# Optimization experiments

Hardware: AMD Instinct MI355X
Metric: run time of the kernel (lower is better)

Reference implementation:

```python
import jax, jax.numpy as jnp
import numpy as np

EMBED = 512
HEADS = 8
SCALE = 4
B, N = 2, 2048
DH = EMBED // HEADS
EPS = 1e-5


def _mha(q_in, k_in, v_in, wq, bq, wk, bk, wv, bv, wo, bo, causal):
    Bq, Nq, _ = q_in.shape
    Nk = k_in.shape[1]
    Q = (q_in @ wq + bq).reshape(Bq, Nq, HEADS, DH)
    K = (k_in @ wk + bk).reshape(Bq, Nk, HEADS, DH)
    V = (v_in @ wv + bv).reshape(Bq, Nk, HEADS, DH)
    # scores: [B, H, Nq, Nk]
    scores = jnp.einsum('bqhd,bkhd->bhqk', Q, K) / np.sqrt(DH).astype(np.float32)
    if causal:
        mask = jnp.triu(jnp.full((Nq, Nq), -jnp.inf, dtype=scores.dtype), k=1)
        scores = scores + mask[None, None]
    attn = jax.nn.softmax(scores, axis=-1)
    out = jnp.einsum('bhqk,bkhd->bqhd', attn, V).reshape(Bq, Nq, EMBED)
    return out @ wo + bo


def _ln(x, g, b):
    mu = jnp.mean(x, axis=-1, keepdims=True)
    var = jnp.var(x, axis=-1, keepdims=True)
    return (x - mu) * jax.lax.rsqrt(var + EPS) * g + b


def setup_inputs() -> dict:
    key = jax.random.key(0)
    ks = iter(jax.random.split(key, 32))
    p = lambda *s: 0.02 * jax.random.normal(next(ks), s, dtype=jnp.float32)
    inp = {
        'x': jax.random.normal(next(ks), (B, N, EMBED), dtype=jnp.float32),
        'encoder_output': jax.random.normal(next(ks), (B, N, EMBED), dtype=jnp.float32),
    }
    for pre in ('sa', 'ca'):
        inp[pre + '_wq'] = p(EMBED, EMBED); inp[pre + '_bq'] = jnp.zeros(EMBED)
        inp[pre + '_wk'] = p(EMBED, EMBED); inp[pre + '_bk'] = jnp.zeros(EMBED)
        inp[pre + '_wv'] = p(EMBED, EMBED); inp[pre + '_bv'] = jnp.zeros(EMBED)
        inp[pre + '_wo'] = p(EMBED, EMBED); inp[pre + '_bo'] = jnp.zeros(EMBED)
    for i in (1, 2, 3):
        inp[f'ln{i}_g'] = jnp.ones(EMBED); inp[f'ln{i}_b'] = jnp.zeros(EMBED)
    inp['ff_w1'] = p(EMBED, SCALE * EMBED); inp['ff_b1'] = jnp.zeros(SCALE * EMBED)
    inp['ff_w2'] = p(SCALE * EMBED, EMBED); inp['ff_b2'] = jnp.zeros(EMBED)
    return inp


def reference(x, encoder_output,
              sa_wq, sa_bq, sa_wk, sa_bk, sa_wv, sa_bv, sa_wo, sa_bo,
              ca_wq, ca_bq, ca_wk, ca_bk, ca_wv, ca_bv, ca_wo, ca_bo,
              ln1_g, ln1_b, ln2_g, ln2_b, ln3_g, ln3_b,
              ff_w1, ff_b1, ff_w2, ff_b2):
    x = _mha(x, x, x, sa_wq, sa_bq, sa_wk, sa_bk, sa_wv, sa_bv, sa_wo, sa_bo, True) + x
    x = _ln(x, ln1_g, ln1_b)
    x = _mha(x, encoder_output, encoder_output,
             ca_wq, ca_bq, ca_wk, ca_bk, ca_wv, ca_bv, ca_wo, ca_bo, False) + x
    x = _ln(x, ln2_g, ln2_b)
    h = jax.nn.gelu(x @ ff_w1 + ff_b1, approximate=False)
    x = h @ ff_w2 + ff_b2 + x
    return _ln(x, ln3_g, ln3_b)
```

## Files before the change

### kernel.cpp

```cpp
#include <hip/hip_runtime.h>
#include <hip/hip_bf16.h>

typedef __bf16 bf16x8 __attribute__((ext_vector_type(8)));
typedef float f32x4 __attribute__((ext_vector_type(4)));
typedef unsigned short u16;

#define EMB 512
#define FF 2048
#define MTOT 4096
#define SEQ 2048

__device__ __forceinline__ u16 f2b(float f) {
  return __builtin_bit_cast(u16, (__bf16)f);
}

__device__ __forceinline__ int swz64(int row) { return ((row >> 3) ^ row) & 7; }

__device__ __forceinline__ void gload16(const u16* g, u16* l) {
  __builtin_amdgcn_global_load_lds(
      (const __attribute__((address_space(1))) unsigned int*)g,
      (__attribute__((address_space(3))) unsigned int*)l, 16, 0, 0);
}

__global__ __launch_bounds__(256) void prep_all(
    const float* s0, const float* s1, const float* s2, const float* s3,
    const float* s4, const float* s5, const float* s6, const float* s7,
    const float* s8, const float* s9,
    u16* d0, u16* d1, u16* d2, u16* d3, u16* d4,
    u16* d5, u16* d6, u16* d7, u16* d8, u16* d9,
    const float* x, u16* xb, const float* enc, u16* encb,
    const float* bq1, const float* bk1, const float* bv1, float* bqkv,
    const float* bk2, const float* bv2, float* bkv) {
  int z = blockIdx.z, bx = blockIdx.x, by = blockIdx.y;
  int tid = threadIdx.x;
  if (z >= 10) {
    int fb = by * 64 + bx;
    const float* src = (z == 10) ? x : enc;
    u16* dst = (z == 10) ? xb : encb;
    size_t base = (size_t)fb * 2048 + tid * 8;
    float4 a = *(const float4*)(src + base);
    float4 b = *(const float4*)(src + base + 4);
    uint4 u;
    u.x = f2b(a.x) | ((unsigned)f2b(a.y) << 16);
    u.y = f2b(a.z) | ((unsigned)f2b(a.w) << 16);
    u.z = f2b(b.x) | ((unsigned)f2b(b.y) << 16);
    u.w = f2b(b.z) | ((unsigned)f2b(b.w) << 16);
    *(uint4*)(dst + base) = u;
    return;
  }
  if (z == 0 && bx == 16 && by == 0) {
    for (int i = tid; i < 1536; i += 256)
      bqkv[i] = (i < 512) ? bq1[i] : (i < 1024 ? bk1[i - 512] : bv1[i - 1024]);
    return;
  }
  if (z == 1 && bx == 16 && by == 0) {
    for (int i = tid; i < 1024; i += 256)
      bkv[i] = (i < 512) ? bk2[i] : bv2[i - 512];
    return;
  }
  const float* src; u16* dst; int K, N;
  switch (z) {
    case 0: src = s0; dst = d0; K = 512; N = 512; break;
    case 1: src = s1; dst = d1; K = 512; N = 512; break;
    case 2: src = s2; dst = d2; K = 512; N = 512; break;
    case 3: src = s3; dst = d3; K = 512; N = 512; break;
    case 4: src = s4; dst = d4; K = 512; N = 512; break;
    case 5: src = s5; dst = d5; K = 512; N = 512; break;
    case 6: src = s6; dst = d6; K = 512; N = 512; break;
    case 7: src = s7; dst = d7; K = 512; N = 512; break;
    case 8: src = s8; dst = d8; K = 512; N = 2048; break;
    default: src = s9; dst = d9; K = 2048; N = 512; break;
  }
  int ntl, ktl;
  if (z == 9) { ktl = bx; ntl = by; } else { ntl = bx; ktl = by; }
  if (ntl * 32 >= N || ktl * 32 >= K) return;
  __shared__ float t[32][33];
  int tx = tid & 31, ty = tid >> 5;
  int n0 = ntl * 32, k0 = ktl * 32;
#pragma unroll
  for (int i = 0; i < 4; i++)
    t[ty + i * 8][tx] = src[(size_t)(k0 + ty + i * 8) * N + n0 + tx];
  __syncthreads();
#pragma unroll
  for (int i = 0; i < 4; i++)
    dst[(size_t)(n0 + ty + i * 8) * K + k0 + tx] = f2b(t[tx][ty + i * 8]);
}

template <bool OUTB, bool OUTF, bool RES, bool GELU_>
__global__ __launch_bounds__(256) void gemm_bt(
    const u16* __restrict__ A, const u16* __restrict__ Bt,
    const float* __restrict__ bias, const float* __restrict__ resid,
    u16* __restrict__ outb, float* __restrict__ outf, int K, int Nd) {
  __shared__ u16 As[128 * 32];
  __shared__ u16 Bs[128 * 32];
  int tid = threadIdx.x;
  int lane = tid & 63, w = tid >> 6;
  int g = lane >> 4, li = lane & 15;
  int wr = w >> 1, wc = w & 1;
  int m0 = blockIdx.x * 128, n0 = blockIdx.y * 128;
  int row_s = tid >> 2, ch_s = tid & 3;
  int cs = ch_s ^ ((row_s ^ (row_s >> 2)) & 3);
  const u16* Ap = A + (size_t)(m0 + row_s) * K + cs * 8;
  const u16* Bp = Bt + (size_t)(n0 + row_s) * K + cs * 8;
  size_t step64 = (size_t)64 * K;
  int s2a = (li ^ (li >> 2)) & 3;
  f32x4 acc[4][4] = {};
  for (int k0 = 0; k0 < K; k0 += 32) {
    __syncthreads();
    gload16(Ap + k0, &As[w * 512]);
    gload16(Ap + step64 + k0, &As[2048 + w * 512]);
    gload16(Bp + k0, &Bs[w * 512]);
    gload16(Bp + step64 + k0, &Bs[2048 + w * 512]);
    __syncthreads();
    bf16x8 af[4], bfr[4];
#pragma unroll
    for (int i = 0; i < 4; i++) {
      af[i] = *(const bf16x8*)&As[(wr * 64 + i * 16 + li) * 32 + (g ^ s2a) * 8];
      bfr[i] = *(const bf16x8*)&Bs[(wc * 64 + i * 16 + li) * 32 + (g ^ s2a) * 8];
    }
#pragma unroll
    for (int mi = 0; mi < 4; mi++)
#pragma unroll
      for (int ni = 0; ni < 4; ni++)
        acc[mi][ni] = __builtin_amdgcn_mfma_f32_16x16x32_bf16(af[mi], bfr[ni], acc[mi][ni], 0, 0, 0);
  }
#pragma unroll
  for (int mi = 0; mi < 4; mi++)
#pragma unroll
    for (int ni = 0; ni < 4; ni++) {
      int gn = n0 + wc * 64 + ni * 16 + li;
      float bv = bias[gn];
#pragma unroll
      for (int r = 0; r < 4; r++) {
        int gm = m0 + wr * 64 + mi * 16 + g * 4 + r;
        float v = acc[mi][ni][r] + bv;
        if (RES) v += resid[(size_t)gm * Nd + gn];
        if (GELU_) v = 0.5f * v * (1.0f + erff(v * 0.70710678118654752f));
        if (OUTF) outf[(size_t)gm * Nd + gn] = v;
        if (OUTB) outb[(size_t)gm * Nd + gn] = f2b(v);
      }
    }
}

template <bool CAUSAL>
__global__ __launch_bounds__(256) void attn_fwd(
    const u16* __restrict__ Q, const u16* __restrict__ Kp,
    const u16* __restrict__ Vp, u16* __restrict__ O, int qs, int kvs) {
  __shared__ u16 Ks[64 * 64];
  __shared__ u16 Vt[64 * 64];
  __shared__ u16 Ps[4][16 * 64];
  int tid = threadIdx.x;
  int lane = tid & 63, w = tid >> 6;
  int g = lane >> 4, li = lane & 15;
  int idx = blockIdx.x;
  int bh = idx & 15;
  int qbi = idx >> 4;
  if (CAUSAL) qbi = (SEQ / 64 - 1) - qbi;
  int qb = qbi * 64;
  int b = bh >> 3, h = bh & 7;
  const u16* Qh = Q + (size_t)b * SEQ * qs + h * 64;
  const u16* Kh = Kp + (size_t)b * SEQ * kvs + h * 64;
  const u16* Vh = Vp + (size_t)b * SEQ * kvs + h * 64;
  int qrow = qb + w * 16 + li;
  int q_hi = qb + w * 16 + 15;
  bf16x8 qa[2];
#pragma unroll
  for (int ks = 0; ks < 2; ks++)
    qa[ks] = *(const bf16x8*)&Qh[(size_t)qrow * qs + ks * 32 + g * 8];
  f32x4 o[4] = {};
  float mreg = -1e30f, lreg = 0.f;
  int sk_key = tid >> 2, sk_c = (tid & 3) * 2;
  int sv_k2 = (tid >> 3) * 2, sv_dg = (tid & 7) * 8;
  int kv_end = CAUSAL ? qb + 64 : SEQ;
  for (int kv0 = 0; kv0 < kv_end; kv0 += 64) {
    __syncthreads();
    {
      uint4 ka = *(const uint4*)&Kh[(size_t)(kv0 + sk_key) * kvs + sk_c * 8];
      uint4 kc = *(const uint4*)&Kh[(size_t)(kv0 + sk_key) * kvs + sk_c * 8 + 8];
      int sw = swz64(sk_key);
      *(uint4*)&Ks[sk_key * 64 + ((sk_c ^ sw) * 8)] = ka;
      *(uint4*)&Ks[sk_key * 64 + (((sk_c + 1) ^ sw) * 8)] = kc;
      uint4 v0 = *(const uint4*)&Vh[(size_t)(kv0 + sv_k2) * kvs + sv_dg];
      uint4 v1 = *(const uint4*)&Vh[(size_t)(kv0 + sv_k2 + 1) * kvs + sv_dg];
      const u16* a0 = (const u16*)&v0;
      const u16* a1 = (const u16*)&v1;
#pragma unroll
      for (int jj = 0; jj < 8; jj++) {
        int d = sv_dg + jj;
        unsigned pk = (unsigned)a0[jj] | ((unsigned)a1[jj] << 16);
        *(unsigned*)&Vt[d * 64 + (sv_k2 ^ (swz64(d) << 3))] = pk;
      }
    }
    __syncthreads();
    if (!CAUSAL || kv0 <= q_hi) {
      f32x4 S[4] = {};
#pragma unroll
      for (int nt = 0; nt < 4; nt++) {
        int krow = nt * 16 + li;
        int sw = swz64(krow) << 3;
#pragma unroll
        for (int ks = 0; ks < 2; ks++) {
          bf16x8 kb = *(const bf16x8*)&Ks[krow * 64 + ((ks * 32 + g * 8) ^ sw)];
          S[nt] = __builtin_amdgcn_mfma_f32_16x16x32_bf16(kb, qa[ks], S[nt], 0, 0, 0);
        }
      }
      float pm = -1e30f;
#pragma unroll
      for (int nt = 0; nt < 4; nt++)
#pragma unroll
        for (int r = 0; r < 4; r++) {
          float s = S[nt][r] * 0.125f;
          if (CAUSAL && (kv0 + nt * 16 + g * 4 + r > qrow)) s = -1e30f;
          S[nt][r] = s;
          pm = fmaxf(pm, s);
        }
      pm = fmaxf(pm, __shfl_xor(pm, 16, 64));
      pm = fmaxf(pm, __shfl_xor(pm, 32, 64));
      float nm = fmaxf(mreg, pm);
      float csc = __expf(mreg - nm);
      float rs = 0.f;
#pragma unroll
      for (int nt = 0; nt < 4; nt++)
#pragma unroll
        for (int r = 0; r < 4; r++) {
          float e = __expf(S[nt][r] - nm);
          S[nt][r] = e;
          rs += e;
        }
      rs += __shfl_xor(rs, 16, 64);
      rs += __shfl_xor(rs, 32, 64);
      lreg = lreg * csc + rs;
      mreg = nm;
      float cscr[4];
#pragma unroll
      for (int r = 0; r < 4; r++)
        cscr[r] = __shfl(csc, (lane & 48) | (g * 4 + r), 64);
#pragma unroll
      for (int nt = 0; nt < 4; nt++)
#pragma unroll
        for (int r = 0; r < 4; r++) o[nt][r] *= cscr[r];
      int swp = swz64(li) << 3;
      u16* pw = Ps[w];
#pragma unroll
      for (int nt = 0; nt < 4; nt++)
#pragma unroll
        for (int rp = 0; rp < 2; rp++) {
          unsigned pk = (unsigned)f2b(S[nt][2 * rp]) |
                        ((unsigned)f2b(S[nt][2 * rp + 1]) << 16);
          *(unsigned*)&pw[li * 64 + ((nt * 16 + g * 4 + 2 * rp) ^ swp)] = pk;
        }
      bf16x8 pa[2];
#pragma unroll
      for (int k2 = 0; k2 < 2; k2++)
        pa[k2] = *(const bf16x8*)&pw[li * 64 + ((k2 * 32 + g * 8) ^ swp)];
#pragma unroll
      for (int nd = 0; nd < 4; nd++) {
        int drow = nd * 16 + li;
        int swv = swz64(drow) << 3;
#pragma unroll
        for (int k2 = 0; k2 < 2; k2++) {
          bf16x8 vb = *(const bf16x8*)&Vt[drow * 64 + ((k2 * 32 + g * 8) ^ swv)];
          o[nd] = __builtin_amdgcn_mfma_f32_16x16x32_bf16(pa[k2], vb, o[nd], 0, 0, 0);
        }
      }
    }
  }
  float linv = 1.0f / lreg;
  float invr[4];
#pragma unroll
  for (int r = 0; r < 4; r++)
    invr[r] = __shfl(linv, (lane & 48) | (g * 4 + r), 64);
#pragma unroll
  for (int nd = 0; nd < 4; nd++)
#pragma unroll
    for (int r = 0; r < 4; r++)
      O[(size_t)b * SEQ * EMB + (size_t)(qb + w * 16 + g * 4 + r) * EMB + h * 64 + nd * 16 + li] =
          f2b(o[nd][r] * invr[r]);
}

__global__ __launch_bounds__(256) void ln_fused(
    const float* __restrict__ in, const float* __restrict__ gamma,
    const float* __restrict__ beta, float* __restrict__ outf, u16* __restrict__ outb) {
  int row = blockIdx.x * 4 + (threadIdx.x >> 6);
  int lane = threadIdx.x & 63;
  const float* p = in + (size_t)row * EMB + lane * 8;
  float v[8];
  *(float4*)&v[0] = *(const float4*)p;
  *(float4*)&v[4] = *(const float4*)(p + 4);
  float s = 0.f, q = 0.f;
#pragma unroll
  for (int j = 0; j < 8; j++) { s += v[j]; q += v[j] * v[j]; }
#pragma unroll
  for (int d = 1; d < 64; d <<= 1) {
    s += __shfl_xor(s, d, 64);
    q += __shfl_xor(q, d, 64);
  }
  float mu = s * (1.0f / EMB);
  float var = q * (1.0f / EMB) - mu * mu;
  float rsig = rsqrtf(var + 1e-5f);
  float gg[8], bb[8];
  *(float4*)&gg[0] = *(const float4*)(gamma + lane * 8);
  *(float4*)&gg[4] = *(const float4*)(gamma + lane * 8 + 4);
  *(float4*)&bb[0] = *(const float4*)(beta + lane * 8);
  *(float4*)&bb[4] = *(const float4*)(beta + lane * 8 + 4);
  float o[8];
#pragma unroll
  for (int j = 0; j < 8; j++) o[j] = (v[j] - mu) * rsig * gg[j] + bb[j];
  float* po = outf + (size_t)row * EMB + lane * 8;
  *(float4*)po = *(float4*)&o[0];
  *(float4*)(po + 4) = *(float4*)&o[4];
  if (outb) {
    uint4 u;
    u.x = f2b(o[0]) | ((unsigned)f2b(o[1]) << 16);
    u.y = f2b(o[2]) | ((unsigned)f2b(o[3]) << 16);
    u.z = f2b(o[4]) | ((unsigned)f2b(o[5]) << 16);
    u.w = f2b(o[6]) | ((unsigned)f2b(o[7]) << 16);
    *(uint4*)(outb + (size_t)row * EMB + lane * 8) = u;
  }
}

extern "C" void kernel_launch(void* const* d_in, const int* in_sizes, int n_in,
                              void* d_out, int out_size, void* d_ws, size_t ws_size,
                              hipStream_t stream) {
  const float* x     = (const float*)d_in[0];
  const float* enc   = (const float*)d_in[1];
  const float* sa_wq = (const float*)d_in[2];
  const float* sa_bq = (const float*)d_in[3];
  const float* sa_wk = (const float*)d_in[4];
  const float* sa_bk = (const float*)d_in[5];
  const float* sa_wv = (const float*)d_in[6];
  const float* sa_bv = (const float*)d_in[7];
  const float* sa_wo = (const float*)d_in[8];
  const float* sa_bo = (const float*)d_in[9];
  const float* ca_wq = (const float*)d_in[10];
  const float* ca_bq = (const float*)d_in[11];
  const float* ca_wk = (const float*)d_in[12];
  const float* ca_bk = (const float*)d_in[13];
  const float* ca_wv = (const float*)d_in[14];
  const float* ca_bv = (const float*)d_in[15];
  const float* ca_wo = (const float*)d_in[16];
  const float* ca_bo = (const float*)d_in[17];
  const float* ln1_g = (const float*)d_in[18];
  const float* ln1_b = (const float*)d_in[19];
  const float* ln2_g = (const float*)d_in[20];
  const float* ln2_b = (const float*)d_in[21];
  const float* ln3_g = (const float*)d_in[22];
  const float* ln3_b = (const float*)d_in[23];
  const float* ff_w1 = (const float*)d_in[24];
  const float* ff_b1 = (const float*)d_in[25];
  const float* ff_w2 = (const float*)d_in[26];
  const float* ff_b2 = (const float*)d_in[27];

  char* ws = (char*)d_ws;
  size_t off = 0;
  auto alloc = [&](size_t bytes) {
    void* p = ws + off;
    off = (off + bytes + 255) & ~(size_t)255;
    return p;
  };
  u16* qkvT_sa  = (u16*)alloc((size_t)1536 * EMB * 2);
  u16* oT_sa    = (u16*)alloc((size_t)EMB * EMB * 2);
  u16* qT_ca    = (u16*)alloc((size_t)EMB * EMB * 2);
  u16* kvT_ca   = (u16*)alloc((size_t)1024 * EMB * 2);
  u16* oT_ca    = (u16*)alloc((size_t)EMB * EMB * 2);
  u16* w1T      = (u16*)alloc((size_t)FF * EMB * 2);
  u16* w2T      = (u16*)alloc((size_t)EMB * FF * 2);
  float* bqkv_sa = (float*)alloc(1536 * 4);
  float* bkv_ca  = (float*)alloc(1024 * 4);
  u16* xb    = (u16*)alloc((size_t)MTOT * EMB * 2);
  u16* encb  = (u16*)alloc((size_t)MTOT * EMB * 2);
  u16* qkv   = (u16*)alloc((size_t)MTOT * 1536 * 2);
  u16* attnb = (u16*)alloc((size_t)MTOT * EMB * 2);
  float* t0  = (float*)alloc((size_t)MTOT * EMB * 4);
  float* x1  = (float*)alloc((size_t)MTOT * EMB * 4);
  u16* x1b   = (u16*)alloc((size_t)MTOT * EMB * 2);
  float* x2  = (float*)alloc((size_t)MTOT * EMB * 4);
  u16* x2b   = (u16*)alloc((size_t)MTOT * EMB * 2);
  u16* hbuf  = (u16*)alloc((size_t)MTOT * FF * 2);
  u16* qca  = xb;
  u16* kvca = qkv;

  prep_all<<<dim3(64, 16, 12), 256, 0, stream>>>(
      sa_wq, sa_wk, sa_wv, sa_wo, ca_wq, ca_wk, ca_wv, ca_wo, ff_w1, ff_w2,
      qkvT_sa, qkvT_sa + 512 * EMB, qkvT_sa + 1024 * EMB, oT_sa, qT_ca,
      kvT_ca, kvT_ca + 512 * EMB, oT_ca, w1T, w2T,
      x, xb, enc, encb,
      sa_bq, sa_bk, sa_bv, bqkv_sa, ca_bk, ca_bv, bkv_ca);

  gemm_bt<true, false, false, false><<<dim3(32, 12), 256, 0, stream>>>(
      xb, qkvT_sa, bqkv_sa, nullptr, qkv, nullptr, EMB, 1536);
  attn_fwd<true><<<512, 256, 0, stream>>>(qkv, qkv + 512, qkv + 1024, attnb, 1536, 1536);
  gemm_bt<false, true, true, false><<<dim3(32, 4), 256, 0, stream>>>(
      attnb, oT_sa, sa_bo, x, nullptr, t0, EMB, EMB);
  ln_fused<<<1024, 256, 0, stream>>>(t0, ln1_g, ln1_b, x1, x1b);

  gemm_bt<true, false, false, false><<<dim3(32, 4), 256, 0, stream>>>(
      x1b, qT_ca, ca_bq, nullptr, qca, nullptr, EMB, EMB);
  gemm_bt<true, false, false, false><<<dim3(32, 8), 256, 0, stream>>>(
      encb, kvT_ca, bkv_ca, nullptr, kvca, nullptr, EMB, 1024);
  attn_fwd<false><<<512, 256, 0, stream>>>(qca, kvca, kvca + 512, attnb, EMB, 1024);
  gemm_bt<false, true, true, false><<<dim3(32, 4), 256, 0, stream>>>(
      attnb, oT_ca, ca_bo, x1, nullptr, t0, EMB, EMB);
  ln_fused<<<1024, 256, 0, stream>>>(t0, ln2_g, ln2_b, x2, x2b);

  gemm_bt<true, false, false, true><<<dim3(32, 16), 256, 0, stream>>>(
      x2b, w1T, ff_b1, nullptr, hbuf, nullptr, EMB, FF);
  gemm_bt<false, true, true, false><<<dim3(32, 4), 256, 0, stream>>>(
      hbuf, w2T, ff_b2, x2, nullptr, t0, FF, EMB);
  ln_fused<<<1024, 256, 0, stream>>>(t0, ln3_g, ln3_b, (float*)d_out, nullptr);
}
```

Baseline: 379.4 us.

## Double-buffer GEMM and attention tiles, widen KV block, shrink narrow GEMM tiles

The GEMM now double-buffers its LDS tiles so the next K-slice is loaded while MFMAs run on the current one. It also gains a BM template parameter, and the 512-wide-output GEMMs use 64-row tiles to launch more blocks. Attention moves to 128-key blocks with double-buffered K (async global-to-LDS) and register-staged V, folds the 1/sqrt(d) scale into Q, and raises wave priority around the MFMA sections. Together these aim to hide memory latency and cut per-iteration barrier overhead. The cost is more LDS per block, which may reduce occupancy, plus bf16 rounding of the pre-scaled Q.

```diff
diff --git a/kernel.cpp b/kernel.cpp
--- a/kernel.cpp
+++ b/kernel.cpp
@@ -13,8 +13,6 @@
 __device__ __forceinline__ u16 f2b(float f) {
   return __builtin_bit_cast(u16, (__bf16)f);
 }
-
-__device__ __forceinline__ int swz64(int row) { return ((row >> 3) ^ row) & 7; }
 
 __device__ __forceinline__ void gload16(const u16* g, u16* l) {
   __builtin_amdgcn_global_load_lds(
@@ -86,53 +84,64 @@
     dst[(size_t)(n0 + ty + i * 8) * K + k0 + tx] = f2b(t[tx][ty + i * 8]);
 }
 
-template <bool OUTB, bool OUTF, bool RES, bool GELU_>
+template <int BM, bool OUTB, bool OUTF, bool RES, bool GELU_>
 __global__ __launch_bounds__(256) void gemm_bt(
     const u16* __restrict__ A, const u16* __restrict__ Bt,
     const float* __restrict__ bias, const float* __restrict__ resid,
     u16* __restrict__ outb, float* __restrict__ outf, int K, int Nd) {
-  __shared__ u16 As[128 * 32];
-  __shared__ u16 Bs[128 * 32];
+  constexpr int MI = BM / 32;
+  __shared__ u16 As[2][BM * 32];
+  __shared__ u16 Bs[2][128 * 32];
   int tid = threadIdx.x;
   int lane = tid & 63, w = tid >> 6;
   int g = lane >> 4, li = lane & 15;
   int wr = w >> 1, wc = w & 1;
-  int m0 = blockIdx.x * 128, n0 = blockIdx.y * 128;
+  int m0 = blockIdx.x * BM, n0 = blockIdx.y * 128;
   int row_s = tid >> 2, ch_s = tid & 3;
   int cs = ch_s ^ ((row_s ^ (row_s >> 2)) & 3);
   const u16* Ap = A + (size_t)(m0 + row_s) * K + cs * 8;
   const u16* Bp = Bt + (size_t)(n0 + row_s) * K + cs * 8;
   size_t step64 = (size_t)64 * K;
   int s2a = (li ^ (li >> 2)) & 3;
-  f32x4 acc[4][4] = {};
-  for (int k0 = 0; k0 < K; k0 += 32) {
-    __syncthreads();
-    gload16(Ap + k0, &As[w * 512]);
-    gload16(Ap + step64 + k0, &As[2048 + w * 512]);
-    gload16(Bp + k0, &Bs[w * 512]);
-    gload16(Bp + step64 + k0, &Bs[2048 + w * 512]);
-    __syncthreads();
-    bf16x8 af[4], bfr[4];
-#pragma unroll
-    for (int i = 0; i < 4; i++) {
-      af[i] = *(const bf16x8*)&As[(wr * 64 + i * 16 + li) * 32 + (g ^ s2a) * 8];
-      bfr[i] = *(const bf16x8*)&Bs[(wc * 64 + i * 16 + li) * 32 + (g ^ s2a) * 8];
-    }
-#pragma unroll
-    for (int mi = 0; mi < 4; mi++)
+  f32x4 acc[MI][4] = {};
+  int T = K >> 5;
+  auto stage = [&](int t, int buf) {
+    int k0 = t << 5;
+    u16* Ad = &As[buf][w * 512];
+    u16* Bd = &Bs[buf][w * 512];
+    gload16(Ap + k0, Ad);
+    if constexpr (BM == 128) gload16(Ap + step64 + k0, Ad + 2048);
+    gload16(Bp + k0, Bd);
+    gload16(Bp + step64 + k0, Bd + 2048);
+  };
+  stage(0, 0);
+  __syncthreads();
+  for (int t = 0; t < T; t++) {
+    int cur = t & 1;
+    if (t + 1 < T) stage(t + 1, cur ^ 1);
+    bf16x8 af[MI], bfr[4];
+#pragma unroll
+    for (int i = 0; i < MI; i++)
+      af[i] = *(const bf16x8*)&As[cur][(wr * (BM / 2) + i * 16 + li) * 32 + (g ^ s2a) * 8];
+#pragma unroll
+    for (int i = 0; i < 4; i++)
+      bfr[i] = *(const bf16x8*)&Bs[cur][(wc * 64 + i * 16 + li) * 32 + (g ^ s2a) * 8];
+#pragma unroll
+    for (int mi = 0; mi < MI; mi++)
 #pragma unroll
       for (int ni = 0; ni < 4; ni++)
         acc[mi][ni] = __builtin_amdgcn_mfma_f32_16x16x32_bf16(af[mi], bfr[ni], acc[mi][ni], 0, 0, 0);
-  }
-#pragma unroll
-  for (int mi = 0; mi < 4; mi++)
+    __syncthreads();
+  }
+#pragma unroll
+  for (int mi = 0; mi < MI; mi++)
 #pragma unroll
     for (int ni = 0; ni < 4; ni++) {
       int gn = n0 + wc * 64 + ni * 16 + li;
       float bv = bias[gn];
 #pragma unroll
       for (int r = 0; r < 4; r++) {
-        int gm = m0 + wr * 64 + mi * 16 + g * 4 + r;
+        int gm = m0 + wr * (BM / 2) + mi * 16 + g * 4 + r;
         float v = acc[mi][ni][r] + bv;
         if (RES) v += resid[(size_t)gm * Nd + gn];
         if (GELU_) v = 0.5f * v * (1.0f + erff(v * 0.70710678118654752f));
@@ -146,9 +155,9 @@
 __global__ __launch_bounds__(256) void attn_fwd(
     const u16* __restrict__ Q, const u16* __restrict__ Kp,
     const u16* __restrict__ Vp, u16* __restrict__ O, int qs, int kvs) {
-  __shared__ u16 Ks[64 * 64];
-  __shared__ u16 Vt[64 * 64];
-  __shared__ u16 Ps[4][16 * 64];
+  __shared__ u16 Ks[2][128 * 64];
+  __shared__ u16 Vt[2][64 * 128];
+  __shared__ u16 Ps[4][16 * 128];
   int tid = threadIdx.x;
   int lane = tid & 63, w = tid >> 6;
   int g = lane >> 4, li = lane & 15;
@@ -162,108 +171,138 @@
   const u16* Kh = Kp + (size_t)b * SEQ * kvs + h * 64;
   const u16* Vh = Vp + (size_t)b * SEQ * kvs + h * 64;
   int qrow = qb + w * 16 + li;
-  int q_hi = qb + w * 16 + 15;
   bf16x8 qa[2];
 #pragma unroll
-  for (int ks = 0; ks < 2; ks++)
-    qa[ks] = *(const bf16x8*)&Qh[(size_t)qrow * qs + ks * 32 + g * 8];
+  for (int ks = 0; ks < 2; ks++) {
+    bf16x8 tq = *(const bf16x8*)&Qh[(size_t)qrow * qs + ks * 32 + g * 8];
+#pragma unroll
+    for (int j = 0; j < 8; j++) tq[j] = (__bf16)((float)tq[j] * 0.125f);
+    qa[ks] = tq;
+  }
+  int kcc = lane & 7;
+  const u16* Ksrc[4];
+#pragma unroll
+  for (int j = 0; j < 4; j++) {
+    int row = j * 32 + w * 8 + (lane >> 3);
+    int sw = ((j * 4 + w) ^ (lane >> 3)) & 7;
+    Ksrc[j] = Kh + (size_t)row * kvs + (kcc ^ sw) * 8;
+  }
+  size_t kstep = (size_t)128 * kvs;
+  int kq = tid & 31, dcv = tid >> 5;
+  const u16* Vsrc = Vh + (size_t)(4 * kq) * kvs + dcv * 8;
+  uint4 vr[4];
+  auto stageK = [&](int t, int buf) {
+    size_t o = (size_t)t * kstep;
+    u16* dst = &Ks[buf][w * 512];
+#pragma unroll
+    for (int j = 0; j < 4; j++) gload16(Ksrc[j] + o, dst + j * 2048);
+  };
+  auto loadV = [&](int t) {
+    size_t o = (size_t)t * kstep;
+#pragma unroll
+    for (int kk = 0; kk < 4; kk++)
+      vr[kk] = *(const uint4*)(Vsrc + o + (size_t)kk * kvs);
+  };
+  auto writeV = [&](int buf) {
+    const u16* a0 = (const u16*)&vr[0];
+    const u16* a1 = (const u16*)&vr[1];
+    const u16* a2 = (const u16*)&vr[2];
+    const u16* a3 = (const u16*)&vr[3];
+#pragma unroll
+    for (int jj = 0; jj < 8; jj++) {
+      int d = dcv * 8 + jj;
+      int swv = ((d >> 3) ^ d) & 15;
+      uint2 pk;
+      pk.x = (unsigned)a0[jj] | ((unsigned)a1[jj] << 16);
+      pk.y = (unsigned)a2[jj] | ((unsigned)a3[jj] << 16);
+      *(uint2*)&Vt[buf][d * 128 + ((kq >> 1) ^ swv) * 8 + 4 * (kq & 1)] = pk;
+    }
+  };
+  int T = CAUSAL ? (qb >> 7) + 1 : SEQ / 128;
+  stageK(0, 0);
+  loadV(0);
+  writeV(0);
+  __syncthreads();
   f32x4 o[4] = {};
   float mreg = -1e30f, lreg = 0.f;
-  int sk_key = tid >> 2, sk_c = (tid & 3) * 2;
-  int sv_k2 = (tid >> 3) * 2, sv_dg = (tid & 7) * 8;
-  int kv_end = CAUSAL ? qb + 64 : SEQ;
-  for (int kv0 = 0; kv0 < kv_end; kv0 += 64) {
-    __syncthreads();
-    {
-      uint4 ka = *(const uint4*)&Kh[(size_t)(kv0 + sk_key) * kvs + sk_c * 8];
-      uint4 kc = *(const uint4*)&Kh[(size_t)(kv0 + sk_key) * kvs + sk_c * 8 + 8];
-      int sw = swz64(sk_key);
-      *(uint4*)&Ks[sk_key * 64 + ((sk_c ^ sw) * 8)] = ka;
-      *(uint4*)&Ks[sk_key * 64 + (((sk_c + 1) ^ sw) * 8)] = kc;
-      uint4 v0 = *(const uint4*)&Vh[(size_t)(kv0 + sv_k2) * kvs + sv_dg];
-      uint4 v1 = *(const uint4*)&Vh[(size_t)(kv0 + sv_k2 + 1) * kvs + sv_dg];
-      const u16* a0 = (const u16*)&v0;
-      const u16* a1 = (const u16*)&v1;
-#pragma unroll
-      for (int jj = 0; jj < 8; jj++) {
-        int d = sv_dg + jj;
-        unsigned pk = (unsigned)a0[jj] | ((unsigned)a1[jj] << 16);
-        *(unsigned*)&Vt[d * 64 + (sv_k2 ^ (swz64(d) << 3))] = pk;
+  for (int t = 0; t < T; t++) {
+    int cur = t & 1;
+    if (t + 1 < T) { stageK(t + 1, cur ^ 1); loadV(t + 1); }
+    int kv0 = t << 7;
+    f32x4 S[8] = {};
+    __builtin_amdgcn_s_setprio(1);
+#pragma unroll
+    for (int nt = 0; nt < 8; nt++) {
+      int krow = nt * 16 + li;
+      int sw = ((krow >> 3) ^ krow) & 7;
+#pragma unroll
+      for (int ks = 0; ks < 2; ks++) {
+        bf16x8 kb = *(const bf16x8*)&Ks[cur][krow * 64 + ((ks * 4 + g) ^ sw) * 8];
+        S[nt] = __builtin_amdgcn_mfma_f32_16x16x32_bf16(kb, qa[ks], S[nt], 0, 0, 0);
       }
     }
-    __syncthreads();
-    if (!CAUSAL || kv0 <= q_hi) {
-      f32x4 S[4] = {};
-#pragma unroll
-      for (int nt = 0; nt < 4; nt++) {
-        int krow = nt * 16 + li;
-        int sw = swz64(krow) << 3;
-#pragma unroll
-        for (int ks = 0; ks < 2; ks++) {
-          bf16x8 kb = *(const bf16x8*)&Ks[krow * 64 + ((ks * 32 + g * 8) ^ sw)];
-          S[nt] = __builtin_amdgcn_mfma_f32_16x16x32_bf16(kb, qa[ks], S[nt], 0, 0, 0);
-        }
+    __builtin_amdgcn_s_setprio(0);
+    float pm = -1e30f;
+#pragma unroll
+    for (int nt = 0; nt < 8; nt++)
+#pragma unroll
+      for (int r = 0; r < 4; r++) {
+        float s = S[nt][r];
+        if (CAUSAL && (kv0 + nt * 16 + g * 4 + r > qrow)) s = -1e30f;
+        S[nt][r] = s;
+        pm = fmaxf(pm, s);
       }
-      float pm = -1e30f;
-#pragma unroll
-      for (int nt = 0; nt < 4; nt++)
-#pragma unroll
-        for (int r = 0; r < 4; r++) {
-          float s = S[nt][r] * 0.125f;
-          if (CAUSAL && (kv0 + nt * 16 + g * 4 + r > qrow)) s = -1e30f;
-          S[nt][r] = s;
-          pm = fmaxf(pm, s);
-        }
-      pm = fmaxf(pm, __shfl_xor(pm, 16, 64));
-      pm = fmaxf(pm, __shfl_xor(pm, 32, 64));
-      float nm = fmaxf(mreg, pm);
-      float csc = __expf(mreg - nm);
-      float rs = 0.f;
-#pragma unroll
-      for (int nt = 0; nt < 4; nt++)
-#pragma unroll
-        for (int r = 0; r < 4; r++) {
-          float e = __expf(S[nt][r] - nm);
-          S[nt][r] = e;
-          rs += e;
-        }
-      rs += __shfl_xor(rs, 16, 64);
-      rs += __shfl_xor(rs, 32, 64);
-      lreg = lreg * csc + rs;
-      mreg = nm;
-      float cscr[4];
-#pragma unroll
-      for (int r = 0; r < 4; r++)
-        cscr[r] = __shfl(csc, (lane & 48) | (g * 4 + r), 64);
-#pragma unroll
-      for (int nt = 0; nt < 4; nt++)
-#pragma unroll
-        for (int r = 0; r < 4; r++) o[nt][r] *= cscr[r];
-      int swp = swz64(li) << 3;
-      u16* pw = Ps[w];
-#pragma unroll
-      for (int nt = 0; nt < 4; nt++)
-#pragma unroll
-        for (int rp = 0; rp < 2; rp++) {
-          unsigned pk = (unsigned)f2b(S[nt][2 * rp]) |
-                        ((unsigned)f2b(S[nt][2 * rp + 1]) << 16);
-          *(unsigned*)&pw[li * 64 + ((nt * 16 + g * 4 + 2 * rp) ^ swp)] = pk;
-        }
-      bf16x8 pa[2];
-#pragma unroll
-      for (int k2 = 0; k2 < 2; k2++)
-        pa[k2] = *(const bf16x8*)&pw[li * 64 + ((k2 * 32 + g * 8) ^ swp)];
-#pragma unroll
-      for (int nd = 0; nd < 4; nd++) {
-        int drow = nd * 16 + li;
-        int swv = swz64(drow) << 3;
-#pragma unroll
-        for (int k2 = 0; k2 < 2; k2++) {
-          bf16x8 vb = *(const bf16x8*)&Vt[drow * 64 + ((k2 * 32 + g * 8) ^ swv)];
-          o[nd] = __builtin_amdgcn_mfma_f32_16x16x32_bf16(pa[k2], vb, o[nd], 0, 0, 0);
-        }
+    pm = fmaxf(pm, __shfl_xor(pm, 16, 64));
+    pm = fmaxf(pm, __shfl_xor(pm, 32, 64));
+    float nm = fmaxf(mreg, pm);
+    float csc = __expf(mreg - nm);
+    float rs = 0.f;
+#pragma unroll
+    for (int nt = 0; nt < 8; nt++)
+#pragma unroll
+      for (int r = 0; r < 4; r++) {
+        float e = __expf(S[nt][r] - nm);
+        S[nt][r] = e;
+        rs += e;
+      }
+    rs += __shfl_xor(rs, 16, 64);
+    rs += __shfl_xor(rs, 32, 64);
+    lreg = lreg * csc + rs;
+    mreg = nm;
+#pragma unroll
+    for (int nt = 0; nt < 8; nt++) {
+      int cp = 2 * nt + (g >> 1);
+      uint2 pk;
+      pk.x = (unsigned)f2b(S[nt][0]) | ((unsigned)f2b(S[nt][1]) << 16);
+      pk.y = (unsigned)f2b(S[nt][2]) | ((unsigned)f2b(S[nt][3]) << 16);
+      *(uint2*)&Ps[w][li * 128 + ((cp ^ li) * 8) + 4 * (g & 1)] = pk;
+    }
+    float cscr[4];
+#pragma unroll
+    for (int r = 0; r < 4; r++)
+      cscr[r] = __shfl(csc, (lane & 48) | (g * 4 + r), 64);
+#pragma unroll
+    for (int nd = 0; nd < 4; nd++)
+#pragma unroll
+      for (int r = 0; r < 4; r++) o[nd][r] *= cscr[r];
+    bf16x8 pa[4];
+#pragma unroll
+    for (int k2 = 0; k2 < 4; k2++)
+      pa[k2] = *(const bf16x8*)&Ps[w][li * 128 + (((k2 * 4 + g) ^ li) * 8)];
+    __builtin_amdgcn_s_setprio(1);
+#pragma unroll
+    for (int nd = 0; nd < 4; nd++) {
+      int d = nd * 16 + li;
+      int swv = ((d >> 3) ^ d) & 15;
+#pragma unroll
+      for (int k2 = 0; k2 < 4; k2++) {
+        bf16x8 vb = *(const bf16x8*)&Vt[cur][d * 128 + (((k2 * 4 + g) ^ swv) * 8)];
+        o[nd] = __builtin_amdgcn_mfma_f32_16x16x32_bf16(pa[k2], vb, o[nd], 0, 0, 0);
       }
     }
+    __builtin_amdgcn_s_setprio(0);
+    if (t + 1 < T) writeV(cur ^ 1);
+    __syncthreads();
   }
   float linv = 1.0f / lreg;
   float invr[4];
@@ -387,25 +426,25 @@
       x, xb, enc, encb,
       sa_bq, sa_bk, sa_bv, bqkv_sa, ca_bk, ca_bv, bkv_ca);
 
-  gemm_bt<true, false, false, false><<<dim3(32, 12), 256, 0, stream>>>(
+  gemm_bt<128, true, false, false, false><<<dim3(32, 12), 256, 0, stream>>>(
       xb, qkvT_sa, bqkv_sa, nullptr, qkv, nullptr, EMB, 1536);
   attn_fwd<true><<<512, 256, 0, stream>>>(qkv, qkv + 512, qkv + 1024, attnb, 1536, 1536);
-  gemm_bt<false, true, true, false><<<dim3(32, 4), 256, 0, stream>>>(
+  gemm_bt<64, false, true, true, false><<<dim3(64, 4), 256, 0, stream>>>(
       attnb, oT_sa, sa_bo, x, nullptr, t0, EMB, EMB);
   ln_fused<<<1024, 256, 0, stream>>>(t0, ln1_g, ln1_b, x1, x1b);
 
-  gemm_bt<true, false, false, false><<<dim3(32, 4), 256, 0, stream>>>(
+  gemm_bt<64, true, false, false, false><<<dim3(64, 4), 256, 0, stream>>>(
       x1b, qT_ca, ca_bq, nullptr, qca, nullptr, EMB, EMB);
-  gemm_bt<true, false, false, false><<<dim3(32, 8), 256, 0, stream>>>(
+  gemm_bt<128, true, false, false, false><<<dim3(32, 8), 256, 0, stream>>>(
       encb, kvT_ca, bkv_ca, nullptr, kvca, nullptr, EMB, 1024);
   attn_fwd<false><<<512, 256, 0, stream>>>(qca, kvca, kvca + 512, attnb, EMB, 1024);
-  gemm_bt<false, true, true, false><<<dim3(32, 4), 256, 0, stream>>>(
+  gemm_bt<64, false, true, true, false><<<dim3(64, 4), 256, 0, stream>>>(
       attnb, oT_ca, ca_bo, x1, nullptr, t0, EMB, EMB);
   ln_fused<<<1024, 256, 0, stream>>>(t0, ln2_g, ln2_b, x2, x2b);
 
-  gemm_bt<true, false, false, true><<<dim3(32, 16), 256, 0, stream>>>(
+  gemm_bt<128, true, false, false, true><<<dim3(32, 16), 256, 0, stream>>>(
       x2b, w1T, ff_b1, nullptr, hbuf, nullptr, EMB, FF);
-  gemm_bt<false, true, true, false><<<dim3(32, 4), 256, 0, stream>>>(
+  gemm_bt<64, false, true, true, false><<<dim3(64, 4), 256, 0, stream>>>(
       hbuf, w2T, ff_b2, x2, nullptr, t0, FF, EMB);
   ln_fused<<<1024, 256, 0, stream>>>(t0, ln3_g, ln3_b, (float*)d_out, nullptr);
 }
```

Result: faster. 355.7 us (-6.3%).
